# Kernel optimization log

Hardware: AMD Instinct MI355X
Metric: run time of the kernel (lower is better)

The kernel has to match this reference:

```python
import jax, jax.numpy as jnp
import numpy as np

N_NODES = 100000
N_EDGES = 1000000
HIDDEN = 64
IN_DIM = 4


def setup_inputs() -> dict:
    key = jax.random.key(0)
    ks = jax.random.split(key, 7)
    x = jax.random.normal(ks[0], (N_NODES, IN_DIM), dtype=jnp.float32)
    edges = jax.random.randint(ks[1], (N_EDGES, 2), 0, N_NODES, dtype=jnp.int32)
    W1 = jax.random.normal(ks[2], (IN_DIM, HIDDEN), dtype=jnp.float32) * 0.5
    b1 = jax.random.normal(ks[3], (HIDDEN,), dtype=jnp.float32) * 0.1
    phases = jax.random.normal(ks[4], (N_EDGES,), dtype=jnp.float32) * 0.1
    Wout = jax.random.normal(ks[5], (HIDDEN, 1), dtype=jnp.float32) * 0.1
    bout = jax.random.normal(ks[6], (1,), dtype=jnp.float32) * 0.1
    return {"x": x, "edges": edges, "W1": W1, "b1": b1,
            "phases": phases, "Wout": Wout, "bout": bout}


def reference(x, edges, W1, b1, phases, Wout, bout):
    # h = lin(x): [N, D]
    h = x @ W1 + b1
    u = edges[:, 0]  # [E]
    v = edges[:, 1]  # [E]
    c = jnp.cos(phases)  # [E]
    s = jnp.sin(phases)  # [E]
    hu = h[u]  # [E, D] gather
    hv = h[v]  # [E, D] gather
    # rot only mixes the first two channels; the rest pass through (eye).
    # msg to v: rot @ h[u] -> [c*h0 - s*h1, s*h0 + c*h1, h2, ...]
    msg_v = jnp.concatenate([
        (c * hu[:, 0] - s * hu[:, 1])[:, None],
        (s * hu[:, 0] + c * hu[:, 1])[:, None],
        hu[:, 2:],
    ], axis=1)
    # msg to u: rot.T @ h[v] -> [c*h0 + s*h1, -s*h0 + c*h1, h2, ...]
    msg_u = jnp.concatenate([
        (c * hv[:, 0] + s * hv[:, 1])[:, None],
        (-s * hv[:, 0] + c * hv[:, 1])[:, None],
        hv[:, 2:],
    ], axis=1)
    diffused = jnp.zeros_like(h).at[v].add(msg_v).at[u].add(msg_u)  # scatter-add
    return (h + diffused) @ Wout + bout  # [N, 1]
```

## Files before the change

kernel.cpp:

```cpp
#include <hip/hip_runtime.h>
#include <hip/hip_fp16.h>

#define N_NODES 100000
#define N_EDGES 1000000
#define HIDDEN 64

#define N_RANGES 3
#define C_RANGE 33344
#define N_SLICES 85
#define PAIRS (N_EDGES / 2)
#define PPB ((PAIRS + N_SLICES - 1) / N_SLICES)
#define A_THREADS 1024

__device__ __forceinline__ void compute_consts(
    const float* __restrict__ W1, const float* __restrict__ b1,
    const float* __restrict__ Wout, const float* __restrict__ bout,
    float* kc, int tid) {
    if (tid < 64) {
        float wj = Wout[tid];
        float p0 = W1[0 * HIDDEN + tid] * wj;
        float p1 = W1[1 * HIDDEN + tid] * wj;
        float p2 = W1[2 * HIDDEN + tid] * wj;
        float p3 = W1[3 * HIDDEN + tid] * wj;
        float pb = b1[tid] * wj;
        #pragma unroll
        for (int off = 32; off > 0; off >>= 1) {
            p0 += __shfl_down(p0, off);
            p1 += __shfl_down(p1, off);
            p2 += __shfl_down(p2, off);
            p3 += __shfl_down(p3, off);
            pb += __shfl_down(pb, off);
        }
        if (tid < 4) {
            kc[5 + tid] = W1[tid * HIDDEN + 0];
            kc[9 + tid] = W1[tid * HIDDEN + 1];
        }
        if (tid == 0) {
            kc[0] = p0; kc[1] = p1; kc[2] = p2; kc[3] = p3; kc[4] = pb;
            kc[13] = b1[0]; kc[14] = b1[1];
            kc[15] = Wout[0]; kc[16] = Wout[1];
            kc[17] = bout[0];
        }
    }
}

__device__ __forceinline__ float contrib(
    float4 xe, float cs, float sn_signed,
    float c0, float c1, float c2, float c3, float cb,
    float a0, float a1, float a2, float a3,
    float g0, float g1, float g2, float g3,
    float b10, float b11, float w0, float w1) {
    float h0 = xe.x * a0 + xe.y * a1 + xe.z * a2 + xe.w * a3 + b10;
    float h1 = xe.x * g0 + xe.y * g1 + xe.z * g2 + xe.w * g3 + b11;
    float d  = xe.x * c0 + xe.y * c1 + xe.z * c2 + xe.w * c3 + cb;
    float a  = h0 * w0 + h1 * w1;
    float b  = h0 * w1 - h1 * w0;
    return cs * a + sn_signed * b + (d - a);
}

__device__ __forceinline__ unsigned pack_half2(float x, float y) {
    __half2 h = __floats2half2_rn(x, y);
    return *(unsigned*)&h;
}

__global__ __launch_bounds__(512) void prep_kernel(
    const float4* __restrict__ x4,
    const float* __restrict__ W1, const float* __restrict__ b1,
    const float* __restrict__ Wout, const float* __restrict__ bout,
    float4* __restrict__ tab) {
    __shared__ float kc[18];
    compute_consts(W1, b1, Wout, bout, kc, threadIdx.x);
    __syncthreads();
    int i = blockIdx.x * 512 + threadIdx.x;
    if (i >= N_NODES) return;
    float4 xi = x4[i];
    float h0 = xi.x * kc[5] + xi.y * kc[6]  + xi.z * kc[7]  + xi.w * kc[8]  + kc[13];
    float h1 = xi.x * kc[9] + xi.y * kc[10] + xi.z * kc[11] + xi.w * kc[12] + kc[14];
    float d  = xi.x * kc[0] + xi.y * kc[1]  + xi.z * kc[2]  + xi.w * kc[3]  + kc[4];
    float a  = h0 * kc[15] + h1 * kc[16];
    float b  = h0 * kc[16] - h1 * kc[15];
    tab[i] = make_float4(a, b, d - a, 0.f);
}

__global__ __launch_bounds__(A_THREADS) void range_kernel(
    const int4* __restrict__ epairs, const float2* __restrict__ ppairs,
    const float4* __restrict__ tab, __half* __restrict__ part) {
    __shared__ float bins[C_RANGE];
    const int tid = threadIdx.x;
    const int r = blockIdx.x / N_SLICES;
    const int s = blockIdx.x - r * N_SLICES;

    {
        float4 z = make_float4(0.f, 0.f, 0.f, 0.f);
        float4* b4 = (float4*)bins;
        for (int j = tid; j < C_RANGE / 4; j += A_THREADS) b4[j] = z;
    }
    __syncthreads();

    const int nlo = r * C_RANGE;
    const int pA = s * PPB;
    const int pB = min(pA + PPB, PAIRS);

    #pragma unroll 2
    for (int p = pA + tid; p < pB; p += A_THREADS) {
        int4   ee = epairs[p];
        float2 pp = ppairs[p];

        unsigned jv0 = (unsigned)(ee.y - nlo);
        unsigned ju0 = (unsigned)(ee.x - nlo);
        unsigned jv1 = (unsigned)(ee.w - nlo);
        unsigned ju1 = (unsigned)(ee.z - nlo);
        bool pv0 = jv0 < C_RANGE, pu0 = ju0 < C_RANGE;
        bool pv1 = jv1 < C_RANGE, pu1 = ju1 < C_RANGE;

        float4 tv0s = tab[pv0 ? ee.x : 0];
        float4 tu0s = tab[pu0 ? ee.y : 0];
        float4 tv1s = tab[pv1 ? ee.z : 0];
        float4 tu1s = tab[pu1 ? ee.w : 0];

        float sn0, cs0, sn1, cs1;
        __sincosf(pp.x, &sn0, &cs0);
        __sincosf(pp.y, &sn1, &cs1);

        float tv0 = fmaf(cs0, tv0s.x, fmaf( sn0, tv0s.y, tv0s.z));
        float tu0 = fmaf(cs0, tu0s.x, fmaf(-sn0, tu0s.y, tu0s.z));
        float tv1 = fmaf(cs1, tv1s.x, fmaf( sn1, tv1s.y, tv1s.z));
        float tu1 = fmaf(cs1, tu1s.x, fmaf(-sn1, tu1s.y, tu1s.z));

        if (pv0) atomicAdd(&bins[jv0], tv0);
        if (pu0) atomicAdd(&bins[ju0], tu0);
        if (pv1) atomicAdd(&bins[jv1], tv1);
        if (pu1) atomicAdd(&bins[ju1], tu1);
    }
    __syncthreads();

    uint2* __restrict__ d2 = (uint2*)(part + (size_t)blockIdx.x * C_RANGE);
    const float4* b4 = (const float4*)bins;
    for (int j = tid; j < C_RANGE / 4; j += A_THREADS) {
        float4 v = b4[j];
        d2[j] = make_uint2(pack_half2(v.x, v.y), pack_half2(v.z, v.w));
    }
}

__global__ __launch_bounds__(512) void reduce_kernel(
    const float4* __restrict__ x4,
    const float* __restrict__ W1, const float* __restrict__ b1,
    const float* __restrict__ Wout, const float* __restrict__ bout,
    const __half2* __restrict__ part2, float2* __restrict__ out2) {
    __shared__ float kc[18];
    compute_consts(W1, b1, Wout, bout, kc, threadIdx.x);
    __syncthreads();
    int t = blockIdx.x * 512 + threadIdx.x;
    int i0 = t * 2;
    if (i0 >= N_NODES) return;
    int r = i0 / C_RANGE;
    int j = i0 - r * C_RANGE;
    const __half2* __restrict__ p = part2
        + (size_t)(r * N_SLICES) * (C_RANGE / 2) + (j >> 1);
    float s0 = 0.0f, s1 = 0.0f;
    #pragma unroll 5
    for (int s = 0; s < N_SLICES; s++) {
        float2 v = __half22float2(p[(size_t)s * (C_RANGE / 2)]);
        s0 += v.x; s1 += v.y;
    }
    float4 xa = x4[i0];
    float4 xb = x4[i0 + 1];
    float base = kc[4] + kc[17];
    out2[t] = make_float2(
        s0 + xa.x * kc[0] + xa.y * kc[1] + xa.z * kc[2] + xa.w * kc[3] + base,
        s1 + xb.x * kc[0] + xb.y * kc[1] + xb.z * kc[2] + xb.w * kc[3] + base);
}

__global__ void precompute_kernel(const float* __restrict__ W1,
                                  const float* __restrict__ b1,
                                  const float* __restrict__ Wout,
                                  const float* __restrict__ bout,
                                  float* __restrict__ consts) {
    __shared__ float kc[18];
    compute_consts(W1, b1, Wout, bout, kc, threadIdx.x);
    __syncthreads();
    if (threadIdx.x < 18) consts[threadIdx.x] = kc[threadIdx.x];
}

__global__ void edge_atomic_kernel(const int2* __restrict__ edges,
                                   const float* __restrict__ phases,
                                   const float4* __restrict__ x4,
                                   const float* __restrict__ consts,
                                   float* __restrict__ rep) {
    int e = blockIdx.x * blockDim.x + threadIdx.x;
    if (e >= N_EDGES) return;
    float c0 = consts[0], c1 = consts[1], c2 = consts[2], c3 = consts[3];
    float cb = consts[4];
    float a0 = consts[5], a1 = consts[6], a2 = consts[7], a3 = consts[8];
    float g0 = consts[9], g1 = consts[10], g2 = consts[11], g3 = consts[12];
    float b10 = consts[13], b11 = consts[14], w0 = consts[15], w1 = consts[16];
    int2 ed = edges[e];
    float ph = phases[e];
    float sn, cs;
    __sincosf(ph, &sn, &cs);
    float4 xu = x4[ed.x];
    float4 xv = x4[ed.y];
    atomicAdd(rep + ed.y, contrib(xu, cs,  sn, c0,c1,c2,c3,cb, a0,a1,a2,a3, g0,g1,g2,g3, b10,b11,w0,w1));
    atomicAdd(rep + ed.x, contrib(xv, cs, -sn, c0,c1,c2,c3,cb, a0,a1,a2,a3, g0,g1,g2,g3, b10,b11,w0,w1));
}

__global__ void final_kernel(const float4* __restrict__ x4,
                             const float* __restrict__ consts,
                             const float* __restrict__ rep,
                             float* __restrict__ out) {
    int i = blockIdx.x * blockDim.x + threadIdx.x;
    if (i >= N_NODES) return;
    float4 xi = x4[i];
    out[i] = rep[i] + xi.x * consts[0] + xi.y * consts[1] + xi.z * consts[2]
           + xi.w * consts[3] + consts[4] + consts[17];
}

extern "C" void kernel_launch(void* const* d_in, const int* in_sizes, int n_in,
                              void* d_out, int out_size, void* d_ws, size_t ws_size,
                              hipStream_t stream) {
    const float* x      = (const float*)d_in[0];
    const int*   edges  = (const int*)d_in[1];
    const float* W1     = (const float*)d_in[2];
    const float* b1     = (const float*)d_in[3];
    const float* phases = (const float*)d_in[4];
    const float* Wout   = (const float*)d_in[5];
    const float* bout   = (const float*)d_in[6];
    float* out = (float*)d_out;

    const size_t part_bytes =
        (size_t)N_RANGES * N_SLICES * C_RANGE * sizeof(__half);
    const size_t tab_off   = part_bytes;
    const size_t tab_bytes = (size_t)N_NODES * sizeof(float4);
    const size_t need      = tab_off + tab_bytes;

    if (ws_size >= need) {
        __half* part = (__half*)d_ws;
        float4* tab  = (float4*)((char*)d_ws + tab_off);
        prep_kernel<<<(N_NODES + 511) / 512, 512, 0, stream>>>(
            (const float4*)x, W1, b1, Wout, bout, tab);
        range_kernel<<<N_RANGES * N_SLICES, A_THREADS, 0, stream>>>(
            (const int4*)edges, (const float2*)phases, tab, part);
        reduce_kernel<<<(N_NODES / 2 + 511) / 512, 512, 0, stream>>>(
            (const float4*)x, W1, b1, Wout, bout,
            (const __half2*)part, (float2*)out);
    } else {
        float* consts = (float*)d_ws;
        float* rep    = (float*)((char*)d_ws + 256);
        hipMemsetAsync(rep, 0, N_NODES * sizeof(float), stream);
        precompute_kernel<<<1, 64, 0, stream>>>(W1, b1, Wout, bout, consts);
        edge_atomic_kernel<<<(N_EDGES + 255) / 256, 256, 0, stream>>>(
            (const int2*)edges, phases, (const float4*)x, consts, rep);
        final_kernel<<<(N_NODES + 255) / 256, 256, 0, stream>>>(
            (const float4*)x, consts, rep, out);
    }
}
```

Baseline: 101.4 us.

## Precompute per-edge contributions once in fp16 before range-binned scatter

```diff
diff --git a/kernel.cpp b/kernel.cpp
--- a/kernel.cpp
+++ b/kernel.cpp
@@ -11,6 +11,7 @@
 #define PAIRS (N_EDGES / 2)
 #define PPB ((PAIRS + N_SLICES - 1) / N_SLICES)
 #define A_THREADS 1024
+#define E_THREADS 512
 
 __device__ __forceinline__ void compute_consts(
     const float* __restrict__ W1, const float* __restrict__ b1,
@@ -63,29 +64,47 @@
     return *(unsigned*)&h;
 }
 
-__global__ __launch_bounds__(512) void prep_kernel(
+__global__ __launch_bounds__(E_THREADS) void edge_kernel(
+    const int4* __restrict__ epairs, const float2* __restrict__ ppairs,
     const float4* __restrict__ x4,
     const float* __restrict__ W1, const float* __restrict__ b1,
     const float* __restrict__ Wout, const float* __restrict__ bout,
-    float4* __restrict__ tab) {
+    uint2* __restrict__ t4) {
     __shared__ float kc[18];
     compute_consts(W1, b1, Wout, bout, kc, threadIdx.x);
     __syncthreads();
-    int i = blockIdx.x * 512 + threadIdx.x;
-    if (i >= N_NODES) return;
-    float4 xi = x4[i];
-    float h0 = xi.x * kc[5] + xi.y * kc[6]  + xi.z * kc[7]  + xi.w * kc[8]  + kc[13];
-    float h1 = xi.x * kc[9] + xi.y * kc[10] + xi.z * kc[11] + xi.w * kc[12] + kc[14];
-    float d  = xi.x * kc[0] + xi.y * kc[1]  + xi.z * kc[2]  + xi.w * kc[3]  + kc[4];
-    float a  = h0 * kc[15] + h1 * kc[16];
-    float b  = h0 * kc[16] - h1 * kc[15];
-    tab[i] = make_float4(a, b, d - a, 0.f);
-}
-
-__global__ __launch_bounds__(A_THREADS) void range_kernel(
-    const int4* __restrict__ epairs, const float2* __restrict__ ppairs,
-    const float4* __restrict__ tab, __half* __restrict__ part) {
-    __shared__ float bins[C_RANGE];
+    int p = blockIdx.x * E_THREADS + threadIdx.x;
+    if (p >= PAIRS) return;
+
+    const float c0 = kc[0], c1 = kc[1], c2 = kc[2], c3 = kc[3], cb = kc[4];
+    const float a0 = kc[5], a1 = kc[6], a2 = kc[7], a3 = kc[8];
+    const float g0 = kc[9], g1 = kc[10], g2 = kc[11], g3 = kc[12];
+    const float b10 = kc[13], b11 = kc[14], w0 = kc[15], w1 = kc[16];
+
+    int4   ee = epairs[p];
+    float2 pp = ppairs[p];
+
+    float4 xu0 = x4[ee.x];
+    float4 xv0 = x4[ee.y];
+    float4 xu1 = x4[ee.z];
+    float4 xv1 = x4[ee.w];
+
+    float sn0, cs0, sn1, cs1;
+    __sincosf(pp.x, &sn0, &cs0);
+    __sincosf(pp.y, &sn1, &cs1);
+
+    float tv0 = contrib(xu0, cs0,  sn0, c0,c1,c2,c3,cb, a0,a1,a2,a3, g0,g1,g2,g3, b10,b11,w0,w1);
+    float tu0 = contrib(xv0, cs0, -sn0, c0,c1,c2,c3,cb, a0,a1,a2,a3, g0,g1,g2,g3, b10,b11,w0,w1);
+    float tv1 = contrib(xu1, cs1,  sn1, c0,c1,c2,c3,cb, a0,a1,a2,a3, g0,g1,g2,g3, b10,b11,w0,w1);
+    float tu1 = contrib(xv1, cs1, -sn1, c0,c1,c2,c3,cb, a0,a1,a2,a3, g0,g1,g2,g3, b10,b11,w0,w1);
+
+    t4[p] = make_uint2(pack_half2(tv0, tu0), pack_half2(tv1, tu1));
+}
+
+__global__ __launch_bounds__(A_THREADS) void bin_kernel(
+    const int4* __restrict__ epairs, const uint2* __restrict__ t4,
+    __half* __restrict__ part) {
+    __shared__ __align__(16) float bins[C_RANGE];
     const int tid = threadIdx.x;
     const int r = blockIdx.x / N_SLICES;
     const int s = blockIdx.x - r * N_SLICES;
@@ -103,34 +122,21 @@
 
     #pragma unroll 2
     for (int p = pA + tid; p < pB; p += A_THREADS) {
-        int4   ee = epairs[p];
-        float2 pp = ppairs[p];
+        int4  ee = epairs[p];
+        uint2 tt = t4[p];
+
+        float2 t01 = __half22float2(*(const __half2*)&tt.x);
+        float2 t23 = __half22float2(*(const __half2*)&tt.y);
 
         unsigned jv0 = (unsigned)(ee.y - nlo);
         unsigned ju0 = (unsigned)(ee.x - nlo);
         unsigned jv1 = (unsigned)(ee.w - nlo);
         unsigned ju1 = (unsigned)(ee.z - nlo);
-        bool pv0 = jv0 < C_RANGE, pu0 = ju0 < C_RANGE;
-        bool pv1 = jv1 < C_RANGE, pu1 = ju1 < C_RANGE;
-
-        float4 tv0s = tab[pv0 ? ee.x : 0];
-        float4 tu0s = tab[pu0 ? ee.y : 0];
-        float4 tv1s = tab[pv1 ? ee.z : 0];
-        float4 tu1s = tab[pu1 ? ee.w : 0];
-
-        float sn0, cs0, sn1, cs1;
-        __sincosf(pp.x, &sn0, &cs0);
-        __sincosf(pp.y, &sn1, &cs1);
-
-        float tv0 = fmaf(cs0, tv0s.x, fmaf( sn0, tv0s.y, tv0s.z));
-        float tu0 = fmaf(cs0, tu0s.x, fmaf(-sn0, tu0s.y, tu0s.z));
-        float tv1 = fmaf(cs1, tv1s.x, fmaf( sn1, tv1s.y, tv1s.z));
-        float tu1 = fmaf(cs1, tu1s.x, fmaf(-sn1, tu1s.y, tu1s.z));
-
-        if (pv0) atomicAdd(&bins[jv0], tv0);
-        if (pu0) atomicAdd(&bins[ju0], tu0);
-        if (pv1) atomicAdd(&bins[jv1], tv1);
-        if (pu1) atomicAdd(&bins[ju1], tu1);
+
+        if (jv0 < C_RANGE) atomicAdd(&bins[jv0], t01.x);
+        if (ju0 < C_RANGE) atomicAdd(&bins[ju0], t01.y);
+        if (jv1 < C_RANGE) atomicAdd(&bins[jv1], t23.x);
+        if (ju1 < C_RANGE) atomicAdd(&bins[ju1], t23.y);
     }
     __syncthreads();
 
@@ -229,17 +235,18 @@
 
     const size_t part_bytes =
         (size_t)N_RANGES * N_SLICES * C_RANGE * sizeof(__half);
-    const size_t tab_off   = part_bytes;
-    const size_t tab_bytes = (size_t)N_NODES * sizeof(float4);
-    const size_t need      = tab_off + tab_bytes;
+    const size_t t4_off   = part_bytes;
+    const size_t t4_bytes = (size_t)PAIRS * sizeof(uint2);
+    const size_t need     = t4_off + t4_bytes;
 
     if (ws_size >= need) {
         __half* part = (__half*)d_ws;
-        float4* tab  = (float4*)((char*)d_ws + tab_off);
-        prep_kernel<<<(N_NODES + 511) / 512, 512, 0, stream>>>(
-            (const float4*)x, W1, b1, Wout, bout, tab);
-        range_kernel<<<N_RANGES * N_SLICES, A_THREADS, 0, stream>>>(
-            (const int4*)edges, (const float2*)phases, tab, part);
+        uint2*  t4   = (uint2*)((char*)d_ws + t4_off);
+        edge_kernel<<<(PAIRS + E_THREADS - 1) / E_THREADS, E_THREADS, 0, stream>>>(
+            (const int4*)edges, (const float2*)phases, (const float4*)x,
+            W1, b1, Wout, bout, t4);
+        bin_kernel<<<N_RANGES * N_SLICES, A_THREADS, 0, stream>>>(
+            (const int4*)edges, t4, part);
         reduce_kernel<<<(N_NODES / 2 + 511) / 512, 512, 0, stream>>>(
             (const float4*)x, W1, b1, Wout, bout,
             (const __half2*)part, (float2*)out);
```

After: 109.6 us. +8.1%, slower.
